# Kernel optimization log

Hardware: AMD Instinct MI355X
Metric: run time of the kernel (lower is better)

## Reference

```python
import jax, jax.numpy as jnp
import numpy as np

N_VERTS = 6890
N_JOINTS = 24
SMPL_PARENT = np.array([0, 0, 0, 1, 2, 3, 4, 5, 6, 7, 8, 9, 9, 9, 12, 13, 14, 16, 17, 18, 19, 20, 21], dtype=np.int32)  # parent of joints 1..23


def rodrigues(r):
    """Axis-angle [N,3] -> rotation matrices [N,3,3]."""
    eps = 1e-8
    theta = jnp.linalg.norm(r, axis=-1, keepdims=True) + eps  # [N,1]
    a = r / theta                                             # unit axis [N,3]
    c = jnp.cos(theta)[..., None]                             # [N,1,1]
    s = jnp.sin(theta)[..., None]
    ax, ay, az = a[:, 0], a[:, 1], a[:, 2]
    zero = jnp.zeros_like(ax)
    K = jnp.stack([zero, -az, ay,
                   az, zero, -ax,
                   -ay, ax, zero], axis=-1).reshape(-1, 3, 3)  # skew [N,3,3]
    outer = a[:, :, None] * a[:, None, :]                      # [N,3,3]
    I = jnp.eye(3, dtype=r.dtype)
    return c * I + (1.0 - c) * outer + s * K


def setup_inputs() -> dict:
    key = jax.random.key(0)
    ks = jax.random.split(key, 7)
    B = 512
    pose = jax.random.normal(ks[0], (B, 72), dtype=jnp.float32) * 0.3
    beta = jax.random.normal(ks[1], (B, 10), dtype=jnp.float32)
    v_template = jax.random.normal(ks[2], (N_VERTS, 3), dtype=jnp.float32)
    shapedirs = jax.random.normal(ks[3], (N_VERTS, 3, 10), dtype=jnp.float32) * 0.01
    posedirs = jax.random.normal(ks[4], (N_VERTS, 3, 207), dtype=jnp.float32) * 0.01
    J_regressor = jax.random.uniform(ks[5], (N_JOINTS, N_VERTS), dtype=jnp.float32)
    J_regressor = J_regressor / jnp.sum(J_regressor, axis=1, keepdims=True)
    weights = jax.random.uniform(ks[6], (N_VERTS, N_JOINTS), dtype=jnp.float32)
    weights = weights / jnp.sum(weights, axis=1, keepdims=True)
    parent = jnp.asarray(SMPL_PARENT)
    return {"pose": pose, "beta": beta, "v_template": v_template,
            "shapedirs": shapedirs, "posedirs": posedirs,
            "J_regressor": J_regressor, "weights": weights, "parent": parent}


def smpl_forward(pose, beta, v_template, shapedirs, posedirs, J_regressor, weights, parent):
    B = pose.shape[0]
    dt = pose.dtype
    # shape blendshapes: [6890,3,10] x [B,10] -> [B,6890,3]
    v_shaped = jnp.einsum('vct,bt->bvc', shapedirs, beta) + v_template[None]
    # rest joints: [24,6890] x [B,6890,3] -> [B,24,3]
    J = jnp.einsum('jv,bvc->bjc', J_regressor, v_shaped)
    # axis-angle -> rotmats
    R = rodrigues(pose.reshape(-1, 3)).reshape(B, N_JOINTS, 3, 3)
    # pose blendshapes from non-root rotations minus identity
    lrotmin = (R[:, 1:] - jnp.eye(3, dtype=dt)).reshape(B, 207)
    v_posed = v_shaped + jnp.einsum('vcp,bp->bvc', posedirs, lrotmin)
    # relative joint offsets
    J_rel = jnp.concatenate([J[:, :1], J[:, 1:] - J[:, parent]], axis=1)  # [B,24,3]
    # local 4x4 transforms
    G_local = jnp.concatenate([R, J_rel[:, :, :, None]], axis=-1)        # [B,24,3,4]
    pad_row = jnp.broadcast_to(jnp.array([0., 0., 0., 1.], dtype=dt).reshape(1, 1, 1, 4),
                               (B, N_JOINTS, 1, 4))
    G_local = jnp.concatenate([G_local, pad_row], axis=2)                # [B,24,4,4]
    # accumulate along kinematic chain (fixed 24-joint unrolled loop)
    Gs = [G_local[:, 0]]
    for i in range(1, N_JOINTS):
        Gs.append(jnp.matmul(Gs[int(SMPL_PARENT[i - 1])], G_local[:, i]))
    G = jnp.stack(Gs, axis=1)                                            # [B,24,4,4]
    # subtract rest-pose contribution (only affects last column)
    rest_vec = jnp.concatenate([J, jnp.zeros((B, N_JOINTS, 1), dtype=dt)], axis=2)  # [B,24,4]
    rest = jnp.zeros((B, N_JOINTS, 4, 4), dtype=dt).at[:, :, :, 3].set(
        jnp.einsum('bjxy,bjy->bjx', G, rest_vec))
    G = G - rest
    # linear blend skinning: [6890,24] x [B,24,4,4] -> [B,6890,4,4]
    T = jnp.einsum('vj,bjxy->bvxy', weights, G)
    rest_shape_h = jnp.concatenate([v_posed, jnp.ones((B, N_VERTS, 1), dtype=dt)], axis=-1)
    v = jnp.einsum('bvxy,bvy->bvx', T, rest_shape_h)[:, :, :3]
    return v


def reference(pose, beta, v_template, shapedirs, posedirs, J_regressor, weights, parent):
    return smpl_forward(pose, beta, v_template, shapedirs, posedirs, J_regressor, weights, parent)
```

## Files before the change

### kernel.cpp

```cpp
#include <hip/hip_runtime.h>

#define NV 6890
#define NVP16 6912
#define NJ 24
#define BATCH 512
#define NCOL 20670
#define NCOLP 20736
#define KK 224
#define JCH 864
#define LSTR 197
#define MTB 32

typedef float f4 __attribute__((ext_vector_type(4)));
typedef float f32x4 __attribute__((ext_vector_type(4)));
typedef short bf16x8 __attribute__((ext_vector_type(8)));
typedef unsigned short ushort8 __attribute__((ext_vector_type(8)));


__device__ __forceinline__ unsigned short bf16_rne(float x) {
  union { float f; unsigned u; } c; c.f = x;
  unsigned r = c.u + 0x7fffu + ((c.u >> 16) & 1u);
  return (unsigned short)(r >> 16);
}
__device__ __forceinline__ float bf16lo_f(unsigned u) {
  union { unsigned u; float f; } c; c.u = u << 16; return c.f;
}
__device__ __forceinline__ float bf16hi_f(unsigned u) {
  union { unsigned u; float f; } c; c.u = u & 0xFFFF0000u; return c.f;
}

__global__ void k_pre(const float* __restrict__ Jreg, const float* __restrict__ vtemp,
                      const float* __restrict__ sdirs, const float* __restrict__ pdirs,
                      const float* __restrict__ wgt,
                      float* __restrict__ partial, unsigned short* __restrict__ Bbuf,
                      unsigned short* __restrict__ Wb) {
  int bid = blockIdx.x;
  int tid = threadIdx.x;
  if (bid < 192) {
    int j = bid >> 3, bz = bid & 7;
    float acc[33];
#pragma unroll
    for (int i = 0; i < 33; ++i) acc[i] = 0.f;
    int v0 = bz * JCH;
    int v1 = v0 + JCH; if (v1 > NV) v1 = NV;
    for (int v = v0 + tid; v < v1; v += 256) {
      float w = Jreg[(size_t)j * NV + v];
      const float* vt = vtemp + (size_t)v * 3;
      acc[0] += w * vt[0]; acc[1] += w * vt[1]; acc[2] += w * vt[2];
      const float* sdv = sdirs + (size_t)v * 30;
#pragma unroll
      for (int t = 0; t < 30; ++t) acc[3 + t] += w * sdv[t];
    }
#pragma unroll
    for (int i = 0; i < 33; ++i) {
      float a = acc[i];
#pragma unroll
      for (int s = 32; s > 0; s >>= 1) a += __shfl_xor(a, s, 64);
      acc[i] = a;
    }
    __shared__ float red[4][34];
    int lane = tid & 63, wv = tid >> 6;
    if (lane == 0) {
#pragma unroll
      for (int i = 0; i < 33; ++i) red[wv][i] = acc[i];
    }
    __syncthreads();
    if (tid < 33) {
      float s = red[0][tid] + red[1][tid] + red[2][tid] + red[3][tid];
      partial[((size_t)j * 8 + bz) * 33 + tid] = s;
    }
    return;
  }
  int idx = (bid - 192) * 256 + tid;
  if (idx < NCOLP * 28) {
    int n = idx / 28, k8 = idx % 28;
    int kc = k8 >> 2, h = k8 & 3;
    ushort8 o;
#pragma unroll
    for (int e = 0; e < 8; ++e) {
      int k = k8 * 8 + e;
      float v = 0.f;
      if (n < NCOL) {
        if (k < 207) v = pdirs[(size_t)n * 207 + k];
        else if (k < 217) v = sdirs[(size_t)n * 10 + (k - 207)];
      }
      o[e] = bf16_rne(v);
    }
    size_t dst = ((size_t)(n >> 4) * 7 + kc) * 512 + (size_t)(h * 16 + (n & 15)) * 8;
    *(ushort8*)(Bbuf + dst) = o;
  } else {
    int widx = idx - NCOLP * 28;
    int v = widx >> 2, q = widx & 3;
    ushort8 o = {0, 0, 0, 0, 0, 0, 0, 0};
    if (v < NV && q < 3) {
#pragma unroll
      for (int e = 0; e < 8; ++e) o[e] = bf16_rne(wgt[(size_t)v * 24 + q * 8 + e]);
    }
    *(ushort8*)(Wb + (size_t)v * 32 + q * 8) = o;
  }
}

__global__ void k_batch(const float* __restrict__ pose, const float* __restrict__ beta,
                        const int* __restrict__ parent, const float* __restrict__ partial,
                        unsigned short* __restrict__ Abuf, unsigned short* __restrict__ Amd) {
  int tid = threadIdx.x;
  int g = tid >> 6;
  int j = tid & 63;
  int b = blockIdx.x * 4 + g;
  __shared__ float JS[NJ][33];
  __shared__ float jl[4][NJ][3];
  __shared__ float gl[4][NJ][16];

  {
    ushort8 z = {0, 0, 0, 0, 0, 0, 0, 0};
    *(ushort8*)(Amd + (size_t)blockIdx.x * 2048 + tid * 8) = z;
  }

  for (int i = tid; i < NJ * 33; i += 256) {
    int jj = i / 33, q = i % 33;
    float s = 0.f;
#pragma unroll
    for (int bz = 0; bz < 8; ++bz) s += partial[((size_t)jj * 8 + bz) * 33 + q];
    JS[jj][q] = s;
  }
  __syncthreads();

  float bt[10];
#pragma unroll
  for (int t = 0; t < 10; ++t) bt[t] = beta[b * 10 + t];

  float R[9];
  float Jj[3] = {0.f, 0.f, 0.f};
  if (j < NJ) {
#pragma unroll
    for (int c = 0; c < 3; ++c) {
      float a = JS[j][c];
#pragma unroll
      for (int t = 0; t < 10; ++t) a += JS[j][3 + c * 10 + t] * bt[t];
      Jj[c] = a;
      jl[g][j][c] = a;
    }
    float rx = pose[b * 72 + j * 3 + 0];
    float ry = pose[b * 72 + j * 3 + 1];
    float rz = pose[b * 72 + j * 3 + 2];
    float theta = sqrtf(rx * rx + ry * ry + rz * rz) + 1e-8f;
    float inv = 1.f / theta;
    float ax = rx * inv, ay = ry * inv, az = rz * inv;
    float c = cosf(theta), s = sinf(theta), oc = 1.f - c;
    R[0] = c + oc * ax * ax;      R[1] = oc * ax * ay - s * az; R[2] = oc * ax * az + s * ay;
    R[3] = oc * ax * ay + s * az; R[4] = c + oc * ay * ay;      R[5] = oc * ay * az - s * ax;
    R[6] = oc * ax * az - s * ay; R[7] = oc * ay * az + s * ax; R[8] = c + oc * az * az;
  }
  __syncthreads();

  if (j >= 1 && j < NJ) {
    unsigned short* lr = Abuf + b * KK + (j - 1) * 9;
#pragma unroll
    for (int k = 0; k < 9; ++k)
      lr[k] = bf16_rne(R[k] - ((k == 0 || k == 4 || k == 8) ? 1.f : 0.f));
  }
  if (j >= 32 && j < 42) Abuf[b * KK + 207 + (j - 32)] = bf16_rne(bt[j - 32]);
  if (j >= 42 && j < 49) Abuf[b * KK + 207 + (j - 32)] = 0;

  if (j < NJ) {
    int par = (j == 0) ? 0 : parent[j - 1];
#pragma unroll
    for (int r = 0; r < 3; ++r) {
      gl[g][j][r * 4 + 0] = R[r * 3 + 0];
      gl[g][j][r * 4 + 1] = R[r * 3 + 1];
      gl[g][j][r * 4 + 2] = R[r * 3 + 2];
      gl[g][j][r * 4 + 3] = (j == 0) ? Jj[r] : Jj[r] - jl[g][par][r];
    }
  }
  __syncthreads();

  if (j < NJ) {
    int a[12];
    int n = 0, cur = j;
    while (cur != 0 && n < 12) { a[n++] = cur; cur = parent[cur - 1]; }
    float G[12];
#pragma unroll
    for (int r = 0; r < 3; ++r)
#pragma unroll
      for (int cc = 0; cc < 4; ++cc) G[r * 4 + cc] = gl[g][0][r * 4 + cc];
    for (int i = n - 1; i >= 0; --i) {
      const float* L = gl[g][a[i]];
      float C[12];
#pragma unroll
      for (int r = 0; r < 3; ++r) {
#pragma unroll
        for (int cc = 0; cc < 4; ++cc) {
          float sacc = (cc == 3) ? G[r * 4 + 3] : 0.f;
#pragma unroll
          for (int k = 0; k < 3; ++k) sacc += G[r * 4 + k] * L[k * 4 + cc];
          C[r * 4 + cc] = sacc;
        }
      }
#pragma unroll
      for (int k = 0; k < 12; ++k) G[k] = C[k];
    }
    float Aval[12];
#pragma unroll
    for (int r = 0; r < 3; ++r) {
      Aval[r * 4 + 0] = G[r * 4 + 0];
      Aval[r * 4 + 1] = G[r * 4 + 1];
      Aval[r * 4 + 2] = G[r * 4 + 2];
      Aval[r * 4 + 3] = G[r * 4 + 3] -
                        (G[r * 4 + 0] * jl[g][j][0] + G[r * 4 + 1] * jl[g][j][1] +
                         G[r * 4 + 2] * jl[g][j][2]);
    }
#pragma unroll
    for (int r = 0; r < 3; ++r)
#pragma unroll
      for (int cc = 0; cc < 4; ++cc)
        Amd[(size_t)b * 512 + (r * 4 + cc) * 32 + j] = bf16_rne(Aval[r * 4 + cc]);
  }
}

__launch_bounds__(256, 4)
__global__ void k_gemmskin(const unsigned short* __restrict__ Abuf,
                           const unsigned short* __restrict__ Bbuf,
                           const float* __restrict__ vtemp,
                           const unsigned short* __restrict__ Amd,
                           const unsigned short* __restrict__ Wb,
                           float* __restrict__ out) {
  __shared__ unsigned vp[(MTB / 2) * LSTR];

  int bid = blockIdx.x;
  int lin = (bid & 7) * 216 + (bid >> 3);
  int bx = lin >> 4;
  int by = lin & 15;

  int tid = threadIdx.x;
  int wid = tid >> 6, lane = tid & 63;
  int lo = lane & 15, hi = lane >> 4;
  int n0 = bx * 192;
  int bb0 = by * MTB;

  bf16x8 Af[2][7];
#pragma unroll
  for (int mt = 0; mt < 2; ++mt) {
    const unsigned short* arow = Abuf + (size_t)(bb0 + mt * 16 + lo) * KK + hi * 8;
#pragma unroll
    for (int kc = 0; kc < 7; ++kc)
      Af[mt][kc] = *(const bf16x8*)(arow + kc * 32);
  }

#pragma unroll
  for (int s = 0; s < 3; ++s) {
    int cb = wid * 48 + s * 16;
    const unsigned short* btile = Bbuf + ((size_t)(bx * 12 + wid * 3 + s) * 7) * 512 + lane * 8;
    bf16x8 Bf[7];
#pragma unroll
    for (int kc = 0; kc < 7; ++kc) Bf[kc] = *(const bf16x8*)(btile + kc * 512);
    int gc = n0 + cb + lo;
    float vt = (gc < NCOL) ? vtemp[gc] : 0.f;
#pragma unroll
    for (int mt = 0; mt < 2; ++mt) {
      f32x4 acc = {vt, vt, vt, vt};
#pragma unroll
      for (int kc = 0; kc < 7; ++kc)
        acc = __builtin_amdgcn_mfma_f32_16x16x32_bf16(Af[mt][kc], Bf[kc], acc, 0, 0, 0);
#pragma unroll
      for (int rp = 0; rp < 2; ++rp) {
        unsigned pr = (unsigned)bf16_rne(acc[2 * rp]) |
                      ((unsigned)bf16_rne(acc[2 * rp + 1]) << 16);
        vp[(mt * 8 + hi * 2 + rp) * LSTR + cb + lo] = pr;
      }
    }
  }

  int vloc = wid * 16 + lo;
  int vg = bx * 64 + vloc;
  bool sok = (vg < NV) && (hi < 3);

  bf16x8 Wf = *(const bf16x8*)(Wb + (size_t)vg * 32 + hi * 8);
  bf16x8 A0p[4], A1p[4];
#pragma unroll
  for (int q = 0; q < 4; ++q) {
    int b0 = bb0 + 2 * q;
    A0p[q] = *(const bf16x8*)(Amd + (size_t)b0 * 512 + lo * 32 + hi * 8);
    A1p[q] = *(const bf16x8*)(Amd + ((size_t)b0 + 1) * 512 + lo * 32 + hi * 8);
  }
  __syncthreads();

#pragma unroll
  for (int g = 0; g < 4; ++g) {
    bf16x8 A0[4], A1[4];
    unsigned ux[4], uy[4], uz[4];
#pragma unroll
    for (int q = 0; q < 4; ++q) {
      int p = g * 4 + q;
      if (g == 0) {
        A0[q] = A0p[q];
        A1[q] = A1p[q];
      } else {
        int b0 = bb0 + 2 * p;
        A0[q] = *(const bf16x8*)(Amd + (size_t)b0 * 512 + lo * 32 + hi * 8);
        A1[q] = *(const bf16x8*)(Amd + ((size_t)b0 + 1) * 512 + lo * 32 + hi * 8);
      }
      ux[q] = vp[p * LSTR + 3 * vloc + 0];
      uy[q] = vp[p * LSTR + 3 * vloc + 1];
      uz[q] = vp[p * LSTR + 3 * vloc + 2];
    }
#pragma unroll
    for (int q = 0; q < 4; ++q) {
      int b0 = bb0 + 2 * (g * 4 + q);
      f32x4 z = {0.f, 0.f, 0.f, 0.f};
      f32x4 c0 = __builtin_amdgcn_mfma_f32_16x16x32_bf16(A0[q], Wf, z, 0, 0, 0);
      f32x4 c1 = __builtin_amdgcn_mfma_f32_16x16x32_bf16(A1[q], Wf, z, 0, 0, 0);
      float o0 = c0[0] * bf16lo_f(ux[q]) + c0[1] * bf16lo_f(uy[q]) + c0[2] * bf16lo_f(uz[q]) + c0[3];
      float o1 = c1[0] * bf16hi_f(ux[q]) + c1[1] * bf16hi_f(uy[q]) + c1[2] * bf16hi_f(uz[q]) + c1[3];
      if (sok) {
        out[((size_t)b0 * NV + vg) * 3 + hi] = o0;
        out[(((size_t)b0 + 1) * NV + vg) * 3 + hi] = o1;
      }
    }
  }
}

extern "C" void kernel_launch(void* const* d_in, const int* in_sizes, int n_in,
                              void* d_out, int out_size, void* d_ws, size_t ws_size,
                              hipStream_t stream) {
  const float* pose   = (const float*)d_in[0];
  const float* beta   = (const float*)d_in[1];
  const float* vtemp  = (const float*)d_in[2];
  const float* sdirs  = (const float*)d_in[3];
  const float* pdirs  = (const float*)d_in[4];
  const float* Jreg   = (const float*)d_in[5];
  const float* wgt    = (const float*)d_in[6];
  const int*   parent = (const int*)d_in[7];
  float* out = (float*)d_out;

  char* wsb = (char*)d_ws;
  unsigned short* Abuf = (unsigned short*)wsb;
  unsigned short* Bbuf = (unsigned short*)(wsb + 229376);
  unsigned short* Amd  = (unsigned short*)(wsb + 9519104);
  float* part          = (float*)(wsb + 10043392);
  unsigned short* Wb   = (unsigned short*)(wsb + 10068736);

  hipLaunchKernelGGL(k_pre, dim3(192 + (NCOLP * 28 + NVP16 * 4) / 256), dim3(256), 0, stream,
                     Jreg, vtemp, sdirs, pdirs, wgt, part, Bbuf, Wb);
  hipLaunchKernelGGL(k_batch, dim3(BATCH / 4), dim3(256), 0, stream, pose, beta, parent, part,
                     Abuf, Amd);
  hipLaunchKernelGGL(k_gemmskin, dim3(1728), dim3(256), 0, stream,
                     Abuf, Bbuf, vtemp, Amd, Wb, out);
}
```

Measured before the change: 57.22 us.

## Process two batch tiles per block and software-pipeline Amd loads

Each k_gemmskin block now handles two consecutive 32-row batch tiles, so the grid is halved to 864 blocks. The per-vertex weight fragment and vtemp values are loaded once and reused across both tiles. The skinning loop now prefetches the next group's Amd fragments while computing the current group, hiding global load latency. In exchange there is an extra barrier between tiles, higher register pressure, and fewer blocks to spread across CUs.

```diff
diff --git a/kernel.cpp b/kernel.cpp
--- a/kernel.cpp
+++ b/kernel.cpp
@@ -227,94 +227,110 @@
   __shared__ unsigned vp[(MTB / 2) * LSTR];
 
   int bid = blockIdx.x;
-  int lin = (bid & 7) * 216 + (bid >> 3);
-  int bx = lin >> 4;
-  int by = lin & 15;
+  int lin = (bid & 7) * 108 + (bid >> 3);
+  int bx = lin >> 3;
+  int byq = lin & 7;
 
   int tid = threadIdx.x;
   int wid = tid >> 6, lane = tid & 63;
   int lo = lane & 15, hi = lane >> 4;
   int n0 = bx * 192;
-  int bb0 = by * MTB;
-
-  bf16x8 Af[2][7];
-#pragma unroll
-  for (int mt = 0; mt < 2; ++mt) {
-    const unsigned short* arow = Abuf + (size_t)(bb0 + mt * 16 + lo) * KK + hi * 8;
-#pragma unroll
-    for (int kc = 0; kc < 7; ++kc)
-      Af[mt][kc] = *(const bf16x8*)(arow + kc * 32);
-  }
-
+
+  float vts[3];
 #pragma unroll
   for (int s = 0; s < 3; ++s) {
-    int cb = wid * 48 + s * 16;
-    const unsigned short* btile = Bbuf + ((size_t)(bx * 12 + wid * 3 + s) * 7) * 512 + lane * 8;
-    bf16x8 Bf[7];
-#pragma unroll
-    for (int kc = 0; kc < 7; ++kc) Bf[kc] = *(const bf16x8*)(btile + kc * 512);
-    int gc = n0 + cb + lo;
-    float vt = (gc < NCOL) ? vtemp[gc] : 0.f;
-#pragma unroll
-    for (int mt = 0; mt < 2; ++mt) {
-      f32x4 acc = {vt, vt, vt, vt};
-#pragma unroll
-      for (int kc = 0; kc < 7; ++kc)
-        acc = __builtin_amdgcn_mfma_f32_16x16x32_bf16(Af[mt][kc], Bf[kc], acc, 0, 0, 0);
-#pragma unroll
-      for (int rp = 0; rp < 2; ++rp) {
-        unsigned pr = (unsigned)bf16_rne(acc[2 * rp]) |
-                      ((unsigned)bf16_rne(acc[2 * rp + 1]) << 16);
-        vp[(mt * 8 + hi * 2 + rp) * LSTR + cb + lo] = pr;
-      }
-    }
-  }
-
+    int gc = n0 + wid * 48 + s * 16 + lo;
+    vts[s] = (gc < NCOL) ? vtemp[gc] : 0.f;
+  }
   int vloc = wid * 16 + lo;
   int vg = bx * 64 + vloc;
   bool sok = (vg < NV) && (hi < 3);
-
   bf16x8 Wf = *(const bf16x8*)(Wb + (size_t)vg * 32 + hi * 8);
-  bf16x8 A0p[4], A1p[4];
-#pragma unroll
-  for (int q = 0; q < 4; ++q) {
-    int b0 = bb0 + 2 * q;
-    A0p[q] = *(const bf16x8*)(Amd + (size_t)b0 * 512 + lo * 32 + hi * 8);
-    A1p[q] = *(const bf16x8*)(Amd + ((size_t)b0 + 1) * 512 + lo * 32 + hi * 8);
-  }
-  __syncthreads();
-
-#pragma unroll
-  for (int g = 0; g < 4; ++g) {
-    bf16x8 A0[4], A1[4];
-    unsigned ux[4], uy[4], uz[4];
+
+#pragma unroll
+  for (int e = 0; e < 2; ++e) {
+    int by = byq * 2 + e;
+    int bb0 = by * MTB;
+
+    if (e == 1) __syncthreads();
+
+    bf16x8 Af[2][7];
+#pragma unroll
+    for (int mt = 0; mt < 2; ++mt) {
+      const unsigned short* arow = Abuf + (size_t)(bb0 + mt * 16 + lo) * KK + hi * 8;
+#pragma unroll
+      for (int kc = 0; kc < 7; ++kc)
+        Af[mt][kc] = *(const bf16x8*)(arow + kc * 32);
+    }
+
+#pragma unroll
+    for (int s = 0; s < 3; ++s) {
+      int cb = wid * 48 + s * 16;
+      const unsigned short* btile = Bbuf + ((size_t)(bx * 12 + wid * 3 + s) * 7) * 512 + lane * 8;
+      bf16x8 Bf[7];
+#pragma unroll
+      for (int kc = 0; kc < 7; ++kc) Bf[kc] = *(const bf16x8*)(btile + kc * 512);
+      float vt = vts[s];
+#pragma unroll
+      for (int mt = 0; mt < 2; ++mt) {
+        f32x4 acc = {vt, vt, vt, vt};
+#pragma unroll
+        for (int kc = 0; kc < 7; ++kc)
+          acc = __builtin_amdgcn_mfma_f32_16x16x32_bf16(Af[mt][kc], Bf[kc], acc, 0, 0, 0);
+#pragma unroll
+        for (int rp = 0; rp < 2; ++rp) {
+          unsigned pr = (unsigned)bf16_rne(acc[2 * rp]) |
+                        ((unsigned)bf16_rne(acc[2 * rp + 1]) << 16);
+          vp[(mt * 8 + hi * 2 + rp) * LSTR + cb + lo] = pr;
+        }
+      }
+    }
+
+    bf16x8 A0c[4], A1c[4];
 #pragma unroll
     for (int q = 0; q < 4; ++q) {
-      int p = g * 4 + q;
-      if (g == 0) {
-        A0[q] = A0p[q];
-        A1[q] = A1p[q];
-      } else {
-        int b0 = bb0 + 2 * p;
-        A0[q] = *(const bf16x8*)(Amd + (size_t)b0 * 512 + lo * 32 + hi * 8);
-        A1[q] = *(const bf16x8*)(Amd + ((size_t)b0 + 1) * 512 + lo * 32 + hi * 8);
-      }
-      ux[q] = vp[p * LSTR + 3 * vloc + 0];
-      uy[q] = vp[p * LSTR + 3 * vloc + 1];
-      uz[q] = vp[p * LSTR + 3 * vloc + 2];
-    }
-#pragma unroll
-    for (int q = 0; q < 4; ++q) {
-      int b0 = bb0 + 2 * (g * 4 + q);
-      f32x4 z = {0.f, 0.f, 0.f, 0.f};
-      f32x4 c0 = __builtin_amdgcn_mfma_f32_16x16x32_bf16(A0[q], Wf, z, 0, 0, 0);
-      f32x4 c1 = __builtin_amdgcn_mfma_f32_16x16x32_bf16(A1[q], Wf, z, 0, 0, 0);
-      float o0 = c0[0] * bf16lo_f(ux[q]) + c0[1] * bf16lo_f(uy[q]) + c0[2] * bf16lo_f(uz[q]) + c0[3];
-      float o1 = c1[0] * bf16hi_f(ux[q]) + c1[1] * bf16hi_f(uy[q]) + c1[2] * bf16hi_f(uz[q]) + c1[3];
-      if (sok) {
-        out[((size_t)b0 * NV + vg) * 3 + hi] = o0;
-        out[(((size_t)b0 + 1) * NV + vg) * 3 + hi] = o1;
-      }
+      int b0 = bb0 + 2 * q;
+      A0c[q] = *(const bf16x8*)(Amd + (size_t)b0 * 512 + lo * 32 + hi * 8);
+      A1c[q] = *(const bf16x8*)(Amd + ((size_t)b0 + 1) * 512 + lo * 32 + hi * 8);
+    }
+    __syncthreads();
+
+#pragma unroll
+    for (int g = 0; g < 4; ++g) {
+      bf16x8 A0n[4], A1n[4];
+      if (g < 3) {
+#pragma unroll
+        for (int q = 0; q < 4; ++q) {
+          int b0 = bb0 + 2 * ((g + 1) * 4 + q);
+          A0n[q] = *(const bf16x8*)(Amd + (size_t)b0 * 512 + lo * 32 + hi * 8);
+          A1n[q] = *(const bf16x8*)(Amd + ((size_t)b0 + 1) * 512 + lo * 32 + hi * 8);
+        }
+      }
+      unsigned ux[4], uy[4], uz[4];
+#pragma unroll
+      for (int q = 0; q < 4; ++q) {
+        int p = g * 4 + q;
+        ux[q] = vp[p * LSTR + 3 * vloc + 0];
+        uy[q] = vp[p * LSTR + 3 * vloc + 1];
+        uz[q] = vp[p * LSTR + 3 * vloc + 2];
+      }
+#pragma unroll
+      for (int q = 0; q < 4; ++q) {
+        int b0 = bb0 + 2 * (g * 4 + q);
+        f32x4 z = {0.f, 0.f, 0.f, 0.f};
+        f32x4 c0 = __builtin_amdgcn_mfma_f32_16x16x32_bf16(A0c[q], Wf, z, 0, 0, 0);
+        f32x4 c1 = __builtin_amdgcn_mfma_f32_16x16x32_bf16(A1c[q], Wf, z, 0, 0, 0);
+        float o0 = c0[0] * bf16lo_f(ux[q]) + c0[1] * bf16lo_f(uy[q]) +
+                   c0[2] * bf16lo_f(uz[q]) + c0[3];
+        float o1 = c1[0] * bf16hi_f(ux[q]) + c1[1] * bf16hi_f(uy[q]) +
+                   c1[2] * bf16hi_f(uz[q]) + c1[3];
+        if (sok) {
+          out[((size_t)b0 * NV + vg) * 3 + hi] = o0;
+          out[(((size_t)b0 + 1) * NV + vg) * 3 + hi] = o1;
+        }
+      }
+#pragma unroll
+      for (int q = 0; q < 4; ++q) { A0c[q] = A0n[q]; A1c[q] = A1n[q]; }
     }
   }
 }
@@ -343,6 +359,6 @@
                      Jreg, vtemp, sdirs, pdirs, wgt, part, Bbuf, Wb);
   hipLaunchKernelGGL(k_batch, dim3(BATCH / 4), dim3(256), 0, stream, pose, beta, parent, part,
                      Abuf, Amd);
-  hipLaunchKernelGGL(k_gemmskin, dim3(1728), dim3(256), 0, stream,
+  hipLaunchKernelGGL(k_gemmskin, dim3(864), dim3(256), 0, stream,
                      Abuf, Bbuf, vtemp, Amd, Wb, out);
 }
```

Measured after the change: 60.88 us. 6.4% more time.

## Use 32x32x16 MFMA for skinning with repacked weights and transform layouts

Applied to the files above, without the earlier changes.

Switches the skinning stage from 16x16x32 MFMAs over pairs of batches to 32x32x16 MFMAs that process two batches in one instruction. Joint weights and per-batch transforms are repacked into 32-row fragment layouts to match. The gemm-skin block drops to 128 threads, each wave owning 96 posed columns, and each wave uses its own shared-memory slice with no block barrier. The aim is fewer MFMA issues, fewer wasted lanes and software-prefetched transform loads. The cost is lower per-block parallelism and more store predication.

```diff
diff --git a/kernel.cpp b/kernel.cpp
--- a/kernel.cpp
+++ b/kernel.cpp
@@ -8,11 +8,12 @@
 #define NCOLP 20736
 #define KK 224
 #define JCH 864
-#define LSTR 197
+#define PSTR 104
 #define MTB 32
 
 typedef float f4 __attribute__((ext_vector_type(4)));
 typedef float f32x4 __attribute__((ext_vector_type(4)));
+typedef float f32x16 __attribute__((ext_vector_type(16)));
 typedef short bf16x8 __attribute__((ext_vector_type(8)));
 typedef unsigned short ushort8 __attribute__((ext_vector_type(8)));
 
@@ -33,7 +34,7 @@
                       const float* __restrict__ sdirs, const float* __restrict__ pdirs,
                       const float* __restrict__ wgt,
                       float* __restrict__ partial, unsigned short* __restrict__ Bbuf,
-                      unsigned short* __restrict__ Wb) {
+                      unsigned short* __restrict__ Wb2) {
   int bid = blockIdx.x;
   int tid = threadIdx.x;
   if (bid < 192) {
@@ -96,13 +97,16 @@
 #pragma unroll
       for (int e = 0; e < 8; ++e) o[e] = bf16_rne(wgt[(size_t)v * 24 + q * 8 + e]);
     }
-    *(ushort8*)(Wb + (size_t)v * 32 + q * 8) = o;
+    int km = q >> 1;
+    int lhalf = q & 1;
+    size_t dst = ((size_t)(v >> 5) * 2 + km) * 512 + (size_t)((v & 31) + 32 * lhalf) * 8;
+    *(ushort8*)(Wb2 + dst) = o;
   }
 }
 
 __global__ void k_batch(const float* __restrict__ pose, const float* __restrict__ beta,
                         const int* __restrict__ parent, const float* __restrict__ partial,
-                        unsigned short* __restrict__ Abuf, unsigned short* __restrict__ Amd) {
+                        unsigned short* __restrict__ Abuf, unsigned short* __restrict__ Amd2) {
   int tid = threadIdx.x;
   int g = tid >> 6;
   int j = tid & 63;
@@ -113,7 +117,7 @@
 
   {
     ushort8 z = {0, 0, 0, 0, 0, 0, 0, 0};
-    *(ushort8*)(Amd + (size_t)blockIdx.x * 2048 + tid * 8) = z;
+    *(ushort8*)(Amd2 + (size_t)blockIdx.x * 2048 + tid * 8) = z;
   }
 
   for (int i = tid; i < NJ * 33; i += 256) {
@@ -209,22 +213,28 @@
                         (G[r * 4 + 0] * jl[g][j][0] + G[r * 4 + 1] * jl[g][j][1] +
                          G[r * 4 + 2] * jl[g][j][2]);
     }
+    int pair = b >> 1, odd = b & 1;
+    int km = j >> 4, kl = j & 15;
+    int lhalf = kl >> 3, e = kl & 7;
+    unsigned short* base = Amd2 + ((size_t)pair * 2 + km) * 512;
 #pragma unroll
     for (int r = 0; r < 3; ++r)
 #pragma unroll
-      for (int cc = 0; cc < 4; ++cc)
-        Amd[(size_t)b * 512 + (r * 4 + cc) * 32 + j] = bf16_rne(Aval[r * 4 + cc]);
-  }
-}
-
-__launch_bounds__(256, 4)
+      for (int cc = 0; cc < 4; ++cc) {
+        int row = odd * 16 + r * 4 + cc;
+        base[(row + 32 * lhalf) * 8 + e] = bf16_rne(Aval[r * 4 + cc]);
+      }
+  }
+}
+
+__launch_bounds__(128, 4)
 __global__ void k_gemmskin(const unsigned short* __restrict__ Abuf,
                            const unsigned short* __restrict__ Bbuf,
                            const float* __restrict__ vtemp,
-                           const unsigned short* __restrict__ Amd,
-                           const unsigned short* __restrict__ Wb,
+                           const unsigned short* __restrict__ Amd2,
+                           const unsigned short* __restrict__ Wb2,
                            float* __restrict__ out) {
-  __shared__ unsigned vp[(MTB / 2) * LSTR];
+  __shared__ unsigned vp[2 * 16 * PSTR];
 
   int bid = blockIdx.x;
   int lin = (bid & 7) * 216 + (bid >> 3);
@@ -232,10 +242,10 @@
   int by = lin & 15;
 
   int tid = threadIdx.x;
-  int wid = tid >> 6, lane = tid & 63;
+  int w = tid >> 6, lane = tid & 63;
   int lo = lane & 15, hi = lane >> 4;
-  int n0 = bx * 192;
   int bb0 = by * MTB;
+  unsigned* wvp = vp + w * 16 * PSTR;
 
   bf16x8 Af[2][7];
 #pragma unroll
@@ -247,13 +257,12 @@
   }
 
 #pragma unroll
-  for (int s = 0; s < 3; ++s) {
-    int cb = wid * 48 + s * 16;
-    const unsigned short* btile = Bbuf + ((size_t)(bx * 12 + wid * 3 + s) * 7) * 512 + lane * 8;
+  for (int s = 0; s < 6; ++s) {
+    const unsigned short* btile = Bbuf + ((size_t)(bx * 12 + w * 6 + s) * 7) * 512 + lane * 8;
     bf16x8 Bf[7];
 #pragma unroll
     for (int kc = 0; kc < 7; ++kc) Bf[kc] = *(const bf16x8*)(btile + kc * 512);
-    int gc = n0 + cb + lo;
+    int gc = bx * 192 + w * 96 + s * 16 + lo;
     float vt = (gc < NCOL) ? vtemp[gc] : 0.f;
 #pragma unroll
     for (int mt = 0; mt < 2; ++mt) {
@@ -265,57 +274,57 @@
       for (int rp = 0; rp < 2; ++rp) {
         unsigned pr = (unsigned)bf16_rne(acc[2 * rp]) |
                       ((unsigned)bf16_rne(acc[2 * rp + 1]) << 16);
-        vp[(mt * 8 + hi * 2 + rp) * LSTR + cb + lo] = pr;
-      }
-    }
-  }
-
-  int vloc = wid * 16 + lo;
-  int vg = bx * 64 + vloc;
-  bool sok = (vg < NV) && (hi < 3);
-
-  bf16x8 Wf = *(const bf16x8*)(Wb + (size_t)vg * 32 + hi * 8);
-  bf16x8 A0p[4], A1p[4];
-#pragma unroll
-  for (int q = 0; q < 4; ++q) {
-    int b0 = bb0 + 2 * q;
-    A0p[q] = *(const bf16x8*)(Amd + (size_t)b0 * 512 + lo * 32 + hi * 8);
-    A1p[q] = *(const bf16x8*)(Amd + ((size_t)b0 + 1) * 512 + lo * 32 + hi * 8);
-  }
-  __syncthreads();
-
-#pragma unroll
-  for (int g = 0; g < 4; ++g) {
-    bf16x8 A0[4], A1[4];
-    unsigned ux[4], uy[4], uz[4];
-#pragma unroll
-    for (int q = 0; q < 4; ++q) {
-      int p = g * 4 + q;
-      if (g == 0) {
-        A0[q] = A0p[q];
-        A1[q] = A1p[q];
-      } else {
-        int b0 = bb0 + 2 * p;
-        A0[q] = *(const bf16x8*)(Amd + (size_t)b0 * 512 + lo * 32 + hi * 8);
-        A1[q] = *(const bf16x8*)(Amd + ((size_t)b0 + 1) * 512 + lo * 32 + hi * 8);
-      }
-      ux[q] = vp[p * LSTR + 3 * vloc + 0];
-      uy[q] = vp[p * LSTR + 3 * vloc + 1];
-      uz[q] = vp[p * LSTR + 3 * vloc + 2];
-    }
-#pragma unroll
-    for (int q = 0; q < 4; ++q) {
-      int b0 = bb0 + 2 * (g * 4 + q);
-      f32x4 z = {0.f, 0.f, 0.f, 0.f};
-      f32x4 c0 = __builtin_amdgcn_mfma_f32_16x16x32_bf16(A0[q], Wf, z, 0, 0, 0);
-      f32x4 c1 = __builtin_amdgcn_mfma_f32_16x16x32_bf16(A1[q], Wf, z, 0, 0, 0);
-      float o0 = c0[0] * bf16lo_f(ux[q]) + c0[1] * bf16lo_f(uy[q]) + c0[2] * bf16lo_f(uz[q]) + c0[3];
-      float o1 = c1[0] * bf16hi_f(ux[q]) + c1[1] * bf16hi_f(uy[q]) + c1[2] * bf16hi_f(uz[q]) + c1[3];
-      if (sok) {
-        out[((size_t)b0 * NV + vg) * 3 + hi] = o0;
-        out[(((size_t)b0 + 1) * NV + vg) * 3 + hi] = o1;
-      }
-    }
+        wvp[(mt * 8 + hi * 2 + rp) * PSTR + s * 16 + lo] = pr;
+      }
+    }
+  }
+
+  int v = lane & 31, h32 = lane >> 5;
+  int vg = bx * 64 + w * 32 + v;
+  bool sok = vg < NV;
+  int vt32 = bx * 2 + w;
+  bf16x8 Wf0 = *(const bf16x8*)(Wb2 + ((size_t)vt32 * 2 + 0) * 512 + lane * 8);
+  bf16x8 Wf1 = *(const bf16x8*)(Wb2 + ((size_t)vt32 * 2 + 1) * 512 + lane * 8);
+
+  int gp0 = by * 16;
+  bf16x8 A0c = *(const bf16x8*)(Amd2 + ((size_t)gp0 * 2 + 0) * 512 + lane * 8);
+  bf16x8 A1c = *(const bf16x8*)(Amd2 + ((size_t)gp0 * 2 + 1) * 512 + lane * 8);
+
+#pragma unroll 4
+  for (int p = 0; p < 16; ++p) {
+    bf16x8 A0n, A1n;
+    if (p < 15) {
+      size_t t = ((size_t)(gp0 + p + 1)) * 2;
+      A0n = *(const bf16x8*)(Amd2 + t * 512 + lane * 8);
+      A1n = *(const bf16x8*)(Amd2 + (t + 1) * 512 + lane * 8);
+    }
+    unsigned ux = wvp[p * PSTR + 3 * v + 0];
+    unsigned uy = wvp[p * PSTR + 3 * v + 1];
+    unsigned uz = wvp[p * PSTR + 3 * v + 2];
+
+    f32x16 acc = {0.f, 0.f, 0.f, 0.f, 0.f, 0.f, 0.f, 0.f,
+                  0.f, 0.f, 0.f, 0.f, 0.f, 0.f, 0.f, 0.f};
+    acc = __builtin_amdgcn_mfma_f32_32x32x16_bf16(A0c, Wf0, acc, 0, 0, 0);
+    acc = __builtin_amdgcn_mfma_f32_32x32x16_bf16(A1c, Wf1, acc, 0, 0, 0);
+
+    float xe = bf16lo_f(ux), ye = bf16lo_f(uy), ze = bf16lo_f(uz);
+    float xo = bf16hi_f(ux), yo = bf16hi_f(uy), zo = bf16hi_f(uz);
+    float oA = acc[0] * xe + acc[1] * ye + acc[2] * ze + acc[3];
+    float oB = acc[4] * xe + acc[5] * ye + acc[6] * ze + acc[7];
+    float oC = acc[8] * xo + acc[9] * yo + acc[10] * zo + acc[11];
+    float oD = acc[12] * xo + acc[13] * yo + acc[14] * zo + acc[15];
+
+    if (sok) {
+      size_t be = (size_t)(bb0 + 2 * p) * NV + vg;
+      size_t bo = be + NV;
+      out[be * 3 + h32] = oA;
+      out[bo * 3 + h32] = oC;
+      if (h32 == 0) {
+        out[be * 3 + 2] = oB;
+        out[bo * 3 + 2] = oD;
+      }
+    }
+    A0c = A0n; A1c = A1n;
   }
 }
 
@@ -335,14 +344,14 @@
   char* wsb = (char*)d_ws;
   unsigned short* Abuf = (unsigned short*)wsb;
   unsigned short* Bbuf = (unsigned short*)(wsb + 229376);
-  unsigned short* Amd  = (unsigned short*)(wsb + 9519104);
+  unsigned short* Amd2 = (unsigned short*)(wsb + 9519104);
   float* part          = (float*)(wsb + 10043392);
-  unsigned short* Wb   = (unsigned short*)(wsb + 10068736);
+  unsigned short* Wb2  = (unsigned short*)(wsb + 10068736);
 
   hipLaunchKernelGGL(k_pre, dim3(192 + (NCOLP * 28 + NVP16 * 4) / 256), dim3(256), 0, stream,
-                     Jreg, vtemp, sdirs, pdirs, wgt, part, Bbuf, Wb);
+                     Jreg, vtemp, sdirs, pdirs, wgt, part, Bbuf, Wb2);
   hipLaunchKernelGGL(k_batch, dim3(BATCH / 4), dim3(256), 0, stream, pose, beta, parent, part,
-                     Abuf, Amd);
-  hipLaunchKernelGGL(k_gemmskin, dim3(1728), dim3(256), 0, stream,
-                     Abuf, Bbuf, vtemp, Amd, Wb, out);
-}
+                     Abuf, Amd2);
+  hipLaunchKernelGGL(k_gemmskin, dim3(1728), dim3(128), 0, stream,
+                     Abuf, Bbuf, vtemp, Amd2, Wb2, out);
+}
```

New measurement: 48.49 us, median of 2. 15.3% less time.
